# Kernel optimization log

Measured on AMD Instinct MI355X. Metric: run time of the kernel, lower is better.

## Reference

```python
import jax, jax.numpy as jnp
import numpy as np

B, T, D, H = 64, 1024, 64, 128  # batch, time, n_mels, gru hidden


def _gru_dir(xW, Whh, bhh, reverse):
    # xW: [B, T, 3H] precomputed input projection; PyTorch gate order: r, z, n
    def step(h, gi):
        gh = h @ Whh.T + bhh
        i_r, i_z, i_n = jnp.split(gi, 3, axis=-1)
        h_r, h_z, h_n = jnp.split(gh, 3, axis=-1)
        r = jax.nn.sigmoid(i_r + h_r)
        zg = jax.nn.sigmoid(i_z + h_z)
        n = jnp.tanh(i_n + r * h_n)
        h2 = (1.0 - zg) * n + zg * h
        return h2, h2
    h0 = jnp.zeros((xW.shape[0], Whh.shape[1]), xW.dtype)
    _, hs = jax.lax.scan(step, h0, jnp.swapaxes(xW, 0, 1), reverse=reverse)
    return jnp.swapaxes(hs, 0, 1)  # [B, T, H]


def _bigru_layer(x, wih_f, whh_f, bih_f, bhh_f, wih_b, whh_b, bih_b, bhh_b):
    hf = _gru_dir(x @ wih_f.T + bih_f, whh_f, bhh_f, False)
    hb = _gru_dir(x @ wih_b.T + bih_b, whh_b, bhh_b, True)
    return jnp.concatenate([hf, hb], axis=-1)  # [B, T, 2H]


def setup_inputs():
    key = jax.random.key(0)
    ks = jax.random.split(key, 24)
    s = 1.0 / np.sqrt(H)  # PyTorch GRU/Linear-ish uniform init scale

    def p(k, shape):
        return jax.random.uniform(k, shape, jnp.float32, -s, s)

    inp = {}
    inp["x"] = jax.random.normal(ks[0], (B, T, D), jnp.float32)
    inp["motor_k"] = jax.random.randint(ks[1], (B,), 0, 5)  # 0-based motor id
    i = 2
    for l, din in [(0, D), (1, 2 * H)]:
        for d in ("f", "b"):
            inp[f"wih_l{l}{d}"] = p(ks[i], (3 * H, din)); i += 1
            inp[f"whh_l{l}{d}"] = p(ks[i], (3 * H, H)); i += 1
            inp[f"bih_l{l}{d}"] = p(ks[i], (3 * H,)); i += 1
            inp[f"bhh_l{l}{d}"] = p(ks[i], (3 * H,)); i += 1
    inp["attn_w"] = p(ks[i], (1, 2 * H)); i += 1
    inp["attn_b"] = jnp.zeros((1,), jnp.float32)
    inp["motor_w"] = p(ks[i], (5, 2 * H)); i += 1
    inp["motor_b"] = jnp.zeros((5,), jnp.float32)
    inp["state_w"] = p(ks[i], (5, 2, 2 * H)); i += 1  # 5 heads, 2 codes each
    inp["state_b"] = jnp.zeros((5, 2), jnp.float32)
    return inp


def reference(x, motor_k,
              wih_l0f, whh_l0f, bih_l0f, bhh_l0f,
              wih_l0b, whh_l0b, bih_l0b, bhh_l0b,
              wih_l1f, whh_l1f, bih_l1f, bhh_l1f,
              wih_l1b, whh_l1b, bih_l1b, bhh_l1b,
              attn_w, attn_b, motor_w, motor_b, state_w, state_b):
    # bi-GRU, 2 layers (dropout inactive at eval)
    z = _bigru_layer(x, wih_l0f, whh_l0f, bih_l0f, bhh_l0f,
                     wih_l0b, whh_l0b, bih_l0b, bhh_l0b)
    z = _bigru_layer(z, wih_l1f, whh_l1f, bih_l1f, bhh_l1f,
                     wih_l1b, whh_l1b, bih_l1b, bhh_l1b)
    # mean-attention pooling over time
    scores = jnp.einsum('btd,od->bt', z, attn_w) + attn_b[0]
    a = jax.nn.softmax(scores, axis=1)
    pooled = jnp.einsum('btd,bt->bd', z, a)  # [B, 2H]
    logits_motor = pooled @ motor_w.T + motor_b  # [B, 5]
    # per-sample conditional head dispatch (all heads have 2 codes -> Cmax=2)
    Wk = state_w[motor_k]  # [B, 2, 2H]
    bk = state_b[motor_k]  # [B, 2]
    logits_state = jnp.einsum('bd,bcd->bc', pooled, Wk) + bk
    return (logits_motor, logits_state)
```

## Files before the change

kernel.cpp:

```cpp
#include <hip/hip_runtime.h>


typedef unsigned short u16;

__global__ __launch_bounds__(256) void proj_f32(
    const float* __restrict__ A, const float* __restrict__ Wf, const float* __restrict__ Wb,
    const float* __restrict__ bf_, const float* __restrict__ bb_,
    float* __restrict__ gi, int K, int t0f, int t0b, int lTc, int GB)
{
  const int N = 384;
  int Tc = 1 << lTc;
  int dir = blockIdx.z;
  const float* __restrict__ W    = dir ? Wb  : Wf;
  const float* __restrict__ bias = dir ? bb_ : bf_;
  int t0 = dir ? t0b : t0f;
  float* __restrict__ o = gi + (size_t)dir * GB * Tc * N;

  __shared__ float As[32][64];
  __shared__ float Bs[32][64];

  int tid = threadIdx.x;
  int tx = tid & 15, ty = tid >> 4;
  int m0 = blockIdx.x * 64;
  int n0 = blockIdx.y * 64;

  int srow = tid >> 2;
  int scol = (tid & 3) * 8;

  int mlA = m0 + srow;
  size_t gA = (size_t)(mlA >> lTc) * 1024 + t0 + (mlA & (Tc - 1));
  const float* arow = A + gA * K;
  const float* wrow = W + (size_t)(n0 + srow) * K;

  float acc[4][4];
#pragma unroll
  for (int i = 0; i < 4; i++)
#pragma unroll
    for (int j = 0; j < 4; j++) acc[i][j] = 0.f;

  for (int kk = 0; kk < K; kk += 32) {
    float4 a0 = *(const float4*)(arow + kk + scol);
    float4 a1 = *(const float4*)(arow + kk + scol + 4);
    float4 b0 = *(const float4*)(wrow + kk + scol);
    float4 b1 = *(const float4*)(wrow + kk + scol + 4);
    __syncthreads();
    As[scol + 0][srow] = a0.x; As[scol + 1][srow] = a0.y;
    As[scol + 2][srow] = a0.z; As[scol + 3][srow] = a0.w;
    As[scol + 4][srow] = a1.x; As[scol + 5][srow] = a1.y;
    As[scol + 6][srow] = a1.z; As[scol + 7][srow] = a1.w;
    Bs[scol + 0][srow] = b0.x; Bs[scol + 1][srow] = b0.y;
    Bs[scol + 2][srow] = b0.z; Bs[scol + 3][srow] = b0.w;
    Bs[scol + 4][srow] = b1.x; Bs[scol + 5][srow] = b1.y;
    Bs[scol + 6][srow] = b1.z; Bs[scol + 7][srow] = b1.w;
    __syncthreads();
#pragma unroll
    for (int k = 0; k < 32; k++) {
      float4 av = *(const float4*)&As[k][ty * 4];
      float4 bv = *(const float4*)&Bs[k][tx * 4];
      float am[4] = {av.x, av.y, av.z, av.w};
      float bn[4] = {bv.x, bv.y, bv.z, bv.w};
#pragma unroll
      for (int i = 0; i < 4; i++)
#pragma unroll
        for (int j = 0; j < 4; j++) acc[i][j] = fmaf(am[i], bn[j], acc[i][j]);
    }
  }
#pragma unroll
  for (int i = 0; i < 4; i++) {
    size_t m = (size_t)(m0 + ty * 4 + i);
#pragma unroll
    for (int j = 0; j < 4; j++) {
      int n = n0 + tx * 4 + j;
      o[m * N + n] = acc[i][j] + bias[n];
    }
  }
}

__global__ __launch_bounds__(256, 1) void gru_recur(
    const float* __restrict__ whhf, const float* __restrict__ whhb,
    const float* __restrict__ bhhf, const float* __restrict__ bhhb,
    const float* __restrict__ gi, float* __restrict__ zout,
    float* __restrict__ hstate, int t0f, int t0b, int first, int Tc, int GB)
{
  const int H = 128, G = 384;
  int b   = blockIdx.x >> 1;
  int dir = blockIdx.x & 1;
  const float* __restrict__ whh = dir ? whhb : whhf;
  const float* __restrict__ bhh = dir ? bhhb : bhhf;
  int t0 = dir ? t0b : t0f;
  int tid  = threadIdx.x;
  int i    = tid & 127;
  int half = tid >> 7;

  float wr[64], wz[64], wn[64];
  {
    const float* pr = whh + (size_t)i * H + half * 64;
    const float* pz = whh + (size_t)(H + i) * H + half * 64;
    const float* pn = whh + (size_t)(2 * H + i) * H + half * 64;
#pragma unroll
    for (int k = 0; k < 64; k += 4) {
      float4 vr = *(const float4*)(pr + k);
      float4 vz = *(const float4*)(pz + k);
      float4 vn = *(const float4*)(pn + k);
      wr[k] = vr.x; wr[k+1] = vr.y; wr[k+2] = vr.z; wr[k+3] = vr.w;
      wz[k] = vz.x; wz[k+1] = vz.y; wz[k+2] = vz.z; wz[k+3] = vz.w;
      wn[k] = vn.x; wn[k+1] = vn.y; wn[k+2] = vn.z; wn[k+3] = vn.w;
    }
  }
  float br = bhh[i], bz = bhh[H + i], bn = bhh[2 * H + i];

  __shared__ __align__(16) float hbuf[2][128];
  __shared__ float pbuf[128][3];

  float* hs = hstate + (size_t)(dir * GB + b) * H;
  float h = 0.f;
  if (first) {
    if (tid < H) { hbuf[0][tid] = 0.f; hbuf[1][tid] = 0.f; }
  } else {
    if (tid < H) hbuf[0][tid] = hs[tid];
    if (half == 0) h = hs[i];
  }

  const float* girow = gi + ((size_t)dir * GB + b) * Tc * G;
  float r0r = 0, r0z = 0, r0n = 0, r1r = 0, r1z = 0, r1n = 0;
  if (half == 0) {
    int tt0 = dir ? (Tc - 1) : 0;
    int tt1 = dir ? (Tc - 2) : 1;
    r0r = girow[(size_t)tt0 * G + i];
    r0z = girow[(size_t)tt0 * G + H + i];
    r0n = girow[(size_t)tt0 * G + 2 * H + i];
    r1r = girow[(size_t)tt1 * G + i];
    r1z = girow[(size_t)tt1 * G + H + i];
    r1n = girow[(size_t)tt1 * G + 2 * H + i];
  }
  __syncthreads();

  for (int s = 0; s < Tc; s++) {
    int cur = s & 1;
    float n2r = 0, n2z = 0, n2n = 0;
    if (half == 0 && s < Tc - 2) {
      int tt2 = dir ? (Tc - 3 - s) : (s + 2);
      const float* gp = girow + (size_t)tt2 * G;
      n2r = gp[i]; n2z = gp[H + i]; n2n = gp[2 * H + i];
    }
    float ar = 0.f, az = 0.f, an = 0.f;
    const float* hc = &hbuf[cur][half * 64];
#pragma unroll
    for (int k = 0; k < 64; k += 4) {
      float4 hv = *(const float4*)(hc + k);
      ar = fmaf(wr[k], hv.x, ar);   az = fmaf(wz[k], hv.x, az);   an = fmaf(wn[k], hv.x, an);
      ar = fmaf(wr[k+1], hv.y, ar); az = fmaf(wz[k+1], hv.y, az); an = fmaf(wn[k+1], hv.y, an);
      ar = fmaf(wr[k+2], hv.z, ar); az = fmaf(wz[k+2], hv.z, az); an = fmaf(wn[k+2], hv.z, an);
      ar = fmaf(wr[k+3], hv.w, ar); az = fmaf(wz[k+3], hv.w, az); an = fmaf(wn[k+3], hv.w, an);
    }
    if (half == 1) { pbuf[i][0] = ar; pbuf[i][1] = az; pbuf[i][2] = an; }
    __syncthreads();
    if (half == 0) {
      int tt = dir ? (Tc - 1 - s) : s;
      int t_abs = t0 + tt;
      float grh = ar + pbuf[i][0] + br;
      float gzh = az + pbuf[i][1] + bz;
      float gnh = an + pbuf[i][2] + bn;
      float rg = 1.f / (1.f + __expf(-(r0r + grh)));
      float zg = 1.f / (1.f + __expf(-(r0z + gzh)));
      float npre = r0n + rg * gnh;
      float e  = __expf(-2.f * fabsf(npre));
      float nv = (1.f - e) / (1.f + e);
      nv = (npre < 0.f) ? -nv : nv;
      h = nv + zg * (h - nv);
      hbuf[cur ^ 1][i] = h;
      zout[((size_t)b * 1024 + t_abs) * 256 + dir * H + i] = h;
      r0r = r1r; r0z = r1z; r0n = r1n;
      r1r = n2r; r1z = n2z; r1n = n2n;
    }
    __syncthreads();
  }
  if (half == 0) hs[i] = h;
}

__global__ __launch_bounds__(256) void pool_heads(
    const float* __restrict__ z2, const float* __restrict__ attn_w, const float* __restrict__ attn_b,
    const float* __restrict__ motor_w, const float* __restrict__ motor_b,
    const float* __restrict__ state_w, const float* __restrict__ state_b,
    const int* __restrict__ motor_k, float* __restrict__ out, int bbase)
{
  const int T = 1024, D2 = 256;
  int bl = blockIdx.x;
  int babs = bbase + bl;
  const float* Z = z2 + (size_t)bl * T * D2;
  __shared__ float sc[1024];
  __shared__ float red[8];
  __shared__ float pooled[256];
  int tid = threadIdx.x, lane = tid & 63, wv = tid >> 6;

  float aw0 = attn_w[lane],       aw1 = attn_w[64 + lane];
  float aw2 = attn_w[128 + lane], aw3 = attn_w[192 + lane];
  float ab = attn_b[0];
  for (int t = wv; t < T; t += 4) {
    const float* zr = Z + (size_t)t * D2;
    float s = zr[lane] * aw0 + zr[64 + lane] * aw1
            + zr[128 + lane] * aw2 + zr[192 + lane] * aw3;
#pragma unroll
    for (int off = 32; off; off >>= 1) s += __shfl_down(s, off);
    if (lane == 0) sc[t] = s + ab;
  }
  __syncthreads();

  float m = -3.0e38f;
  for (int t = tid; t < T; t += 256) m = fmaxf(m, sc[t]);
#pragma unroll
  for (int off = 32; off; off >>= 1) m = fmaxf(m, __shfl_down(m, off));
  if (lane == 0) red[wv] = m;
  __syncthreads();
  m = fmaxf(fmaxf(red[0], red[1]), fmaxf(red[2], red[3]));
  float sum = 0.f;
  for (int t = tid; t < T; t += 256) { float e = __expf(sc[t] - m); sc[t] = e; sum += e; }
#pragma unroll
  for (int off = 32; off; off >>= 1) sum += __shfl_down(sum, off);
  if (lane == 0) red[4 + wv] = sum;
  __syncthreads();
  float S = red[4] + red[5] + red[6] + red[7];
  float inv = 1.f / S;

  float acc = 0.f;
  for (int t = 0; t < T; t++) acc = fmaf(sc[t], Z[(size_t)t * D2 + tid], acc);
  pooled[tid] = acc * inv;
  __syncthreads();

  int o = tid >> 5, sl = tid & 31;
  if (o < 7) {
    int mk = motor_k[babs];
    const float* wp; float bias;
    if (o < 5) { wp = motor_w + o * D2;                          bias = motor_b[o]; }
    else       { wp = state_w + ((size_t)mk * 2 + (o - 5)) * D2; bias = state_b[mk * 2 + (o - 5)]; }
    float s = 0.f;
    for (int d = sl; d < D2; d += 32) s += pooled[d] * wp[d];
#pragma unroll
    for (int off = 16; off; off >>= 1) s += __shfl_down(s, off);
    if (sl == 0) {
      float v = s + bias;
      if (o < 5) out[babs * 5 + o] = v;
      else       out[320 + babs * 2 + (o - 5)] = v;
    }
  }
}

extern "C" void kernel_launch(void* const* d_in, const int* in_sizes, int n_in,
                              void* d_out, int out_size, void* d_ws, size_t ws_size,
                              hipStream_t stream) {
  const float* x       = (const float*)d_in[0];
  const int*   motor_k = (const int*)d_in[1];
  const float* wih_l0f = (const float*)d_in[2];
  const float* whh_l0f = (const float*)d_in[3];
  const float* bih_l0f = (const float*)d_in[4];
  const float* bhh_l0f = (const float*)d_in[5];
  const float* wih_l0b = (const float*)d_in[6];
  const float* whh_l0b = (const float*)d_in[7];
  const float* bih_l0b = (const float*)d_in[8];
  const float* bhh_l0b = (const float*)d_in[9];
  const float* wih_l1f = (const float*)d_in[10];
  const float* whh_l1f = (const float*)d_in[11];
  const float* bih_l1f = (const float*)d_in[12];
  const float* bhh_l1f = (const float*)d_in[13];
  const float* wih_l1b = (const float*)d_in[14];
  const float* whh_l1b = (const float*)d_in[15];
  const float* bih_l1b = (const float*)d_in[16];
  const float* bhh_l1b = (const float*)d_in[17];
  const float* attn_w  = (const float*)d_in[18];
  const float* attn_b  = (const float*)d_in[19];
  const float* motor_w = (const float*)d_in[20];
  const float* motor_b = (const float*)d_in[21];
  const float* state_w = (const float*)d_in[22];
  const float* state_b = (const float*)d_in[23];

  static const int candGB[9] = {64,32,16,8,4,2,1,1,1};
  static const int candTc[9] = {256,256,256,256,256,256,256,128,64};
  int GB = 1, Tc = 64;
  for (int c = 0; c < 9; c++) {
    size_t nb = (size_t)candGB[c] * 1024 * 256 * 4 * 2
              + (size_t)2 * candGB[c] * candTc[c] * 384 * 4
              + (size_t)2 * candGB[c] * 128 * 4;
    if (nb <= ws_size) { GB = candGB[c]; Tc = candTc[c]; break; }
  }
  int lTc = 31 - __builtin_clz((unsigned)Tc);
  int nc = 1024 / Tc;

  float* z1 = (float*)d_ws;
  float* z2 = z1 + (size_t)GB * 1024 * 256;
  float* gi = z2 + (size_t)GB * 1024 * 256;
  float* hstate = gi + (size_t)2 * GB * Tc * 384;

  dim3 gpb((unsigned)(GB * Tc / 64), 6, 2);
  for (int gb = 0; gb < 64 / GB; gb++) {
    const float* xg = x + (size_t)gb * GB * 1024 * 64;
    for (int c = 0; c < nc; c++) {
      int t0f = c * Tc, t0b = (nc - 1 - c) * Tc;
      proj_f32<<<gpb, 256, 0, stream>>>(xg, wih_l0f, wih_l0b, bih_l0f, bih_l0b,
                                        gi, 64, t0f, t0b, lTc, GB);
      gru_recur<<<2 * GB, 256, 0, stream>>>(whh_l0f, whh_l0b, bhh_l0f, bhh_l0b, gi, z1,
                                            hstate, t0f, t0b, c == 0, Tc, GB);
    }
    for (int c = 0; c < nc; c++) {
      int t0f = c * Tc, t0b = (nc - 1 - c) * Tc;
      proj_f32<<<gpb, 256, 0, stream>>>(z1, wih_l1f, wih_l1b, bih_l1f, bih_l1b,
                                        gi, 256, t0f, t0b, lTc, GB);
      gru_recur<<<2 * GB, 256, 0, stream>>>(whh_l1f, whh_l1b, bhh_l1f, bhh_l1b, gi, z2,
                                            hstate, t0f, t0b, c == 0, Tc, GB);
    }
    pool_heads<<<GB, 256, 0, stream>>>(z2, attn_w, attn_b, motor_w, motor_b,
                                       state_w, state_b, motor_k, (float*)d_out, gb * GB);
  }
}
```

Measured before the change: 2.234 ms.

## Move GRU pipeline to fp16 with MFMA projection and fdot2 recurrence

Converts the input and input-projection weights to fp16 in a preprocessing kernel. The projection GEMM is replaced by an MFMA 16x16x32 f16 kernel, and gi, z1 and z2 are stored as fp16 to halve memory traffic. The recurrence packs Whh into half2 registers, broadcasts h through readlane and uses fdot2. Both directions of a sample are merged into one 512-thread block. All of this reduces arithmetic and bandwidth cost at the price of fp16 rounding in the hidden state and activations, which may affect accuracy over 1024 steps.

Result: slower. 3.050 ms (+36.5%).

```diff
diff --git a/kernel.cpp b/kernel.cpp
--- a/kernel.cpp
+++ b/kernel.cpp
@@ -2,97 +2,95 @@
 
 
 typedef unsigned short u16;
-
-__global__ __launch_bounds__(256) void proj_f32(
-    const float* __restrict__ A, const float* __restrict__ Wf, const float* __restrict__ Wb,
+typedef _Float16 f16;
+typedef f16  h2  __attribute__((ext_vector_type(2)));
+typedef f16  h8  __attribute__((ext_vector_type(8)));
+typedef float fv4 __attribute__((ext_vector_type(4)));
+
+#if defined(__has_builtin)
+#if __has_builtin(__builtin_amdgcn_fdot2)
+#define HAVE_FDOT2 1
+#endif
+#endif
+
+struct Cvt5 { const float* src[5]; unsigned dst[5]; unsigned cum[6]; };
+
+__global__ void cvt_f16(Cvt5 jb, f16* __restrict__ arena, unsigned total) {
+  unsigned stride = gridDim.x * blockDim.x;
+  for (unsigned idx = blockIdx.x * blockDim.x + threadIdx.x; idx < total; idx += stride) {
+    int j = 0;
+    while (idx >= jb.cum[j + 1]) j++;
+    unsigned e = idx - jb.cum[j];
+    arena[jb.dst[j] + e] = (f16)jb.src[j][e];
+  }
+}
+
+__global__ __launch_bounds__(256) void proj_f16(
+    const f16* __restrict__ A, const f16* __restrict__ Wf, const f16* __restrict__ Wb,
     const float* __restrict__ bf_, const float* __restrict__ bb_,
-    float* __restrict__ gi, int K, int t0f, int t0b, int lTc, int GB)
+    f16* __restrict__ gi, int K, int t0f, int t0b, int lTc, int GB)
 {
   const int N = 384;
   int Tc = 1 << lTc;
-  int dir = blockIdx.z;
-  const float* __restrict__ W    = dir ? Wb  : Wf;
+  int dir = blockIdx.y;
+  const f16* __restrict__ W     = dir ? Wb  : Wf;
   const float* __restrict__ bias = dir ? bb_ : bf_;
   int t0 = dir ? t0b : t0f;
-  float* __restrict__ o = gi + (size_t)dir * GB * Tc * N;
-
-  __shared__ float As[32][64];
-  __shared__ float Bs[32][64];
-
-  int tid = threadIdx.x;
-  int tx = tid & 15, ty = tid >> 4;
-  int m0 = blockIdx.x * 64;
-  int n0 = blockIdx.y * 64;
-
-  int srow = tid >> 2;
-  int scol = (tid & 3) * 8;
-
-  int mlA = m0 + srow;
-  size_t gA = (size_t)(mlA >> lTc) * 1024 + t0 + (mlA & (Tc - 1));
-  const float* arow = A + gA * K;
-  const float* wrow = W + (size_t)(n0 + srow) * K;
-
-  float acc[4][4];
-#pragma unroll
-  for (int i = 0; i < 4; i++)
-#pragma unroll
-    for (int j = 0; j < 4; j++) acc[i][j] = 0.f;
+  f16* __restrict__ o = gi + (size_t)dir * GB * Tc * N;
+
+  int lane = threadIdx.x & 63;
+  int wv   = threadIdx.x >> 6;
+  int mbase = blockIdx.x * 64 + wv * 16;
+  int col  = lane & 15;
+  int koff = (lane >> 4) * 8;
+
+  int ml = mbase + col;
+  size_t g = (size_t)(ml >> lTc) * 1024 + t0 + (ml & (Tc - 1));
+  const f16* ap = A + g * K + koff;
+  const f16* wp = W + (size_t)col * K + koff;
+
+  fv4 acc[24];
+#pragma unroll
+  for (int i = 0; i < 24; i++) acc[i] = (fv4){0.f, 0.f, 0.f, 0.f};
 
   for (int kk = 0; kk < K; kk += 32) {
-    float4 a0 = *(const float4*)(arow + kk + scol);
-    float4 a1 = *(const float4*)(arow + kk + scol + 4);
-    float4 b0 = *(const float4*)(wrow + kk + scol);
-    float4 b1 = *(const float4*)(wrow + kk + scol + 4);
-    __syncthreads();
-    As[scol + 0][srow] = a0.x; As[scol + 1][srow] = a0.y;
-    As[scol + 2][srow] = a0.z; As[scol + 3][srow] = a0.w;
-    As[scol + 4][srow] = a1.x; As[scol + 5][srow] = a1.y;
-    As[scol + 6][srow] = a1.z; As[scol + 7][srow] = a1.w;
-    Bs[scol + 0][srow] = b0.x; Bs[scol + 1][srow] = b0.y;
-    Bs[scol + 2][srow] = b0.z; Bs[scol + 3][srow] = b0.w;
-    Bs[scol + 4][srow] = b1.x; Bs[scol + 5][srow] = b1.y;
-    Bs[scol + 6][srow] = b1.z; Bs[scol + 7][srow] = b1.w;
-    __syncthreads();
-#pragma unroll
-    for (int k = 0; k < 32; k++) {
-      float4 av = *(const float4*)&As[k][ty * 4];
-      float4 bv = *(const float4*)&Bs[k][tx * 4];
-      float am[4] = {av.x, av.y, av.z, av.w};
-      float bn[4] = {bv.x, bv.y, bv.z, bv.w};
-#pragma unroll
-      for (int i = 0; i < 4; i++)
-#pragma unroll
-        for (int j = 0; j < 4; j++) acc[i][j] = fmaf(am[i], bn[j], acc[i][j]);
-    }
-  }
-#pragma unroll
-  for (int i = 0; i < 4; i++) {
-    size_t m = (size_t)(m0 + ty * 4 + i);
-#pragma unroll
-    for (int j = 0; j < 4; j++) {
-      int n = n0 + tx * 4 + j;
-      o[m * N + n] = acc[i][j] + bias[n];
-    }
-  }
-}
-
-__global__ __launch_bounds__(256, 1) void gru_recur(
+    h8 a = *(const h8*)(ap + kk);
+#pragma unroll
+    for (int nt = 0; nt < 24; nt++) {
+      h8 bfrag = *(const h8*)(wp + (size_t)nt * 16 * K + kk);
+      acc[nt] = __builtin_amdgcn_mfma_f32_16x16x32_f16(a, bfrag, acc[nt], 0, 0, 0);
+    }
+  }
+  int rowq = (lane >> 4) * 4;
+#pragma unroll
+  for (int nt = 0; nt < 24; nt++) {
+    int n = nt * 16 + col;
+    float bs = bias[n];
+#pragma unroll
+    for (int r = 0; r < 4; r++) {
+      size_t m = (size_t)(mbase + rowq + r);
+      o[m * N + n] = (f16)(acc[nt][r] + bs);
+    }
+  }
+}
+
+__global__ __launch_bounds__(512, 2) void gru_recur(
     const float* __restrict__ whhf, const float* __restrict__ whhb,
     const float* __restrict__ bhhf, const float* __restrict__ bhhb,
-    const float* __restrict__ gi, float* __restrict__ zout,
+    const f16* __restrict__ gi, f16* __restrict__ zout,
     float* __restrict__ hstate, int t0f, int t0b, int first, int Tc, int GB)
 {
   const int H = 128, G = 384;
-  int b   = blockIdx.x >> 1;
-  int dir = blockIdx.x & 1;
+  int tid  = threadIdx.x;
+  int dir  = tid >> 8;
+  int i    = tid & 127;
+  int half = (tid >> 7) & 1;
+  int b    = blockIdx.x;
   const float* __restrict__ whh = dir ? whhb : whhf;
   const float* __restrict__ bhh = dir ? bhhb : bhhf;
   int t0 = dir ? t0b : t0f;
-  int tid  = threadIdx.x;
-  int i    = tid & 127;
-  int half = tid >> 7;
-
-  float wr[64], wz[64], wn[64];
+
+  h2 wr2[32], wz2[32], wn2[32];
   {
     const float* pr = whh + (size_t)i * H + half * 64;
     const float* pz = whh + (size_t)(H + i) * H + half * 64;
@@ -102,27 +100,29 @@
       float4 vr = *(const float4*)(pr + k);
       float4 vz = *(const float4*)(pz + k);
       float4 vn = *(const float4*)(pn + k);
-      wr[k] = vr.x; wr[k+1] = vr.y; wr[k+2] = vr.z; wr[k+3] = vr.w;
-      wz[k] = vz.x; wz[k+1] = vz.y; wz[k+2] = vz.z; wz[k+3] = vz.w;
-      wn[k] = vn.x; wn[k+1] = vn.y; wn[k+2] = vn.z; wn[k+3] = vn.w;
+      wr2[k/2]     = (h2){(f16)vr.x, (f16)vr.y};
+      wr2[k/2 + 1] = (h2){(f16)vr.z, (f16)vr.w};
+      wz2[k/2]     = (h2){(f16)vz.x, (f16)vz.y};
+      wz2[k/2 + 1] = (h2){(f16)vz.z, (f16)vz.w};
+      wn2[k/2]     = (h2){(f16)vn.x, (f16)vn.y};
+      wn2[k/2 + 1] = (h2){(f16)vn.z, (f16)vn.w};
     }
   }
   float br = bhh[i], bz = bhh[H + i], bn = bhh[2 * H + i];
 
-  __shared__ __align__(16) float hbuf[2][128];
-  __shared__ float pbuf[128][3];
+  __shared__ __align__(16) f16 hbuf2[2][2][128];
+  __shared__ float pbuf[2][128][3];
 
   float* hs = hstate + (size_t)(dir * GB + b) * H;
   float h = 0.f;
-  if (first) {
-    if (tid < H) { hbuf[0][tid] = 0.f; hbuf[1][tid] = 0.f; }
-  } else {
-    if (tid < H) hbuf[0][tid] = hs[tid];
-    if (half == 0) h = hs[i];
-  }
-
-  const float* girow = gi + ((size_t)dir * GB + b) * Tc * G;
-  float r0r = 0, r0z = 0, r0n = 0, r1r = 0, r1z = 0, r1n = 0;
+  if (half == 0) {
+    if (!first) h = hs[i];
+    hbuf2[dir][0][i] = (f16)h;
+  }
+
+  const f16* girow = gi + (size_t)(dir * GB + b) * Tc * G;
+  f16 r0r = (f16)0.f, r0z = (f16)0.f, r0n = (f16)0.f;
+  f16 r1r = (f16)0.f, r1z = (f16)0.f, r1n = (f16)0.f;
   if (half == 0) {
     int tt0 = dir ? (Tc - 1) : 0;
     int tt1 = dir ? (Tc - 2) : 1;
@@ -135,41 +135,52 @@
   }
   __syncthreads();
 
+  int lane = tid & 63;
+  const int* hb[2] = { (const int*)&hbuf2[dir][0][0], (const int*)&hbuf2[dir][1][0] };
+  int hidx = half * 32 + (lane & 31);
+
   for (int s = 0; s < Tc; s++) {
     int cur = s & 1;
-    float n2r = 0, n2z = 0, n2n = 0;
+    f16 n2r = (f16)0.f, n2z = (f16)0.f, n2n = (f16)0.f;
     if (half == 0 && s < Tc - 2) {
       int tt2 = dir ? (Tc - 3 - s) : (s + 2);
-      const float* gp = girow + (size_t)tt2 * G;
+      const f16* gp = girow + (size_t)tt2 * G;
       n2r = gp[i]; n2z = gp[H + i]; n2n = gp[2 * H + i];
     }
+    int hv = hb[cur][hidx];
     float ar = 0.f, az = 0.f, an = 0.f;
-    const float* hc = &hbuf[cur][half * 64];
-#pragma unroll
-    for (int k = 0; k < 64; k += 4) {
-      float4 hv = *(const float4*)(hc + k);
-      ar = fmaf(wr[k], hv.x, ar);   az = fmaf(wz[k], hv.x, az);   an = fmaf(wn[k], hv.x, an);
-      ar = fmaf(wr[k+1], hv.y, ar); az = fmaf(wz[k+1], hv.y, az); an = fmaf(wn[k+1], hv.y, an);
-      ar = fmaf(wr[k+2], hv.z, ar); az = fmaf(wz[k+2], hv.z, az); an = fmaf(wn[k+2], hv.z, an);
-      ar = fmaf(wr[k+3], hv.w, ar); az = fmaf(wz[k+3], hv.w, az); an = fmaf(wn[k+3], hv.w, an);
-    }
-    if (half == 1) { pbuf[i][0] = ar; pbuf[i][1] = az; pbuf[i][2] = an; }
+#pragma unroll
+    for (int k = 0; k < 32; k++) {
+      int si = __builtin_amdgcn_readlane(hv, k);
+      h2 sh; __builtin_memcpy(&sh, &si, 4);
+#if HAVE_FDOT2
+      ar = __builtin_amdgcn_fdot2(wr2[k], sh, ar, false);
+      az = __builtin_amdgcn_fdot2(wz2[k], sh, az, false);
+      an = __builtin_amdgcn_fdot2(wn2[k], sh, an, false);
+#else
+      float s0 = (float)sh[0], s1 = (float)sh[1];
+      ar = fmaf((float)wr2[k][0], s0, ar); ar = fmaf((float)wr2[k][1], s1, ar);
+      az = fmaf((float)wz2[k][0], s0, az); az = fmaf((float)wz2[k][1], s1, az);
+      an = fmaf((float)wn2[k][0], s0, an); an = fmaf((float)wn2[k][1], s1, an);
+#endif
+    }
+    if (half == 1) { pbuf[dir][i][0] = ar; pbuf[dir][i][1] = az; pbuf[dir][i][2] = an; }
     __syncthreads();
     if (half == 0) {
       int tt = dir ? (Tc - 1 - s) : s;
       int t_abs = t0 + tt;
-      float grh = ar + pbuf[i][0] + br;
-      float gzh = az + pbuf[i][1] + bz;
-      float gnh = an + pbuf[i][2] + bn;
-      float rg = 1.f / (1.f + __expf(-(r0r + grh)));
-      float zg = 1.f / (1.f + __expf(-(r0z + gzh)));
-      float npre = r0n + rg * gnh;
+      float grh = ar + pbuf[dir][i][0] + br;
+      float gzh = az + pbuf[dir][i][1] + bz;
+      float gnh = an + pbuf[dir][i][2] + bn;
+      float rg = 1.f / (1.f + __expf(-((float)r0r + grh)));
+      float zg = 1.f / (1.f + __expf(-((float)r0z + gzh)));
+      float npre = (float)r0n + rg * gnh;
       float e  = __expf(-2.f * fabsf(npre));
       float nv = (1.f - e) / (1.f + e);
       nv = (npre < 0.f) ? -nv : nv;
       h = nv + zg * (h - nv);
-      hbuf[cur ^ 1][i] = h;
-      zout[((size_t)b * 1024 + t_abs) * 256 + dir * H + i] = h;
+      hbuf2[dir][cur ^ 1][i] = (f16)h;
+      zout[((size_t)b * 1024 + t_abs) * 256 + dir * H + i] = (f16)h;
       r0r = r1r; r0z = r1z; r0n = r1n;
       r1r = n2r; r1z = n2z; r1n = n2n;
     }
@@ -179,7 +190,7 @@
 }
 
 __global__ __launch_bounds__(256) void pool_heads(
-    const float* __restrict__ z2, const float* __restrict__ attn_w, const float* __restrict__ attn_b,
+    const f16* __restrict__ z2, const float* __restrict__ attn_w, const float* __restrict__ attn_b,
     const float* __restrict__ motor_w, const float* __restrict__ motor_b,
     const float* __restrict__ state_w, const float* __restrict__ state_b,
     const int* __restrict__ motor_k, float* __restrict__ out, int bbase)
@@ -187,7 +198,7 @@
   const int T = 1024, D2 = 256;
   int bl = blockIdx.x;
   int babs = bbase + bl;
-  const float* Z = z2 + (size_t)bl * T * D2;
+  const f16* Z = z2 + (size_t)bl * T * D2;
   __shared__ float sc[1024];
   __shared__ float red[8];
   __shared__ float pooled[256];
@@ -197,9 +208,9 @@
   float aw2 = attn_w[128 + lane], aw3 = attn_w[192 + lane];
   float ab = attn_b[0];
   for (int t = wv; t < T; t += 4) {
-    const float* zr = Z + (size_t)t * D2;
-    float s = zr[lane] * aw0 + zr[64 + lane] * aw1
-            + zr[128 + lane] * aw2 + zr[192 + lane] * aw3;
+    const f16* zr = Z + (size_t)t * D2;
+    float s = (float)zr[lane] * aw0 + (float)zr[64 + lane] * aw1
+            + (float)zr[128 + lane] * aw2 + (float)zr[192 + lane] * aw3;
 #pragma unroll
     for (int off = 32; off; off >>= 1) s += __shfl_down(s, off);
     if (lane == 0) sc[t] = s + ab;
@@ -223,7 +234,7 @@
   float inv = 1.f / S;
 
   float acc = 0.f;
-  for (int t = 0; t < T; t++) acc = fmaf(sc[t], Z[(size_t)t * D2 + tid], acc);
+  for (int t = 0; t < T; t++) acc = fmaf(sc[t], (float)Z[(size_t)t * D2 + tid], acc);
   pooled[tid] = acc * inv;
   __syncthreads();
 
@@ -248,21 +259,16 @@
 extern "C" void kernel_launch(void* const* d_in, const int* in_sizes, int n_in,
                               void* d_out, int out_size, void* d_ws, size_t ws_size,
                               hipStream_t stream) {
-  const float* x       = (const float*)d_in[0];
-  const int*   motor_k = (const int*)d_in[1];
-  const float* wih_l0f = (const float*)d_in[2];
+  const int* motor_k = (const int*)d_in[1];
   const float* whh_l0f = (const float*)d_in[3];
   const float* bih_l0f = (const float*)d_in[4];
   const float* bhh_l0f = (const float*)d_in[5];
-  const float* wih_l0b = (const float*)d_in[6];
   const float* whh_l0b = (const float*)d_in[7];
   const float* bih_l0b = (const float*)d_in[8];
   const float* bhh_l0b = (const float*)d_in[9];
-  const float* wih_l1f = (const float*)d_in[10];
   const float* whh_l1f = (const float*)d_in[11];
   const float* bih_l1f = (const float*)d_in[12];
   const float* bhh_l1f = (const float*)d_in[13];
-  const float* wih_l1b = (const float*)d_in[14];
   const float* whh_l1b = (const float*)d_in[15];
   const float* bih_l1b = (const float*)d_in[16];
   const float* bhh_l1b = (const float*)d_in[17];
@@ -273,39 +279,59 @@
   const float* state_w = (const float*)d_in[22];
   const float* state_b = (const float*)d_in[23];
 
+  static const unsigned nel[5] = {4194304, 24576, 24576, 98304, 98304};
+  static const int      idx[5] = {0, 2, 6, 10, 14};
+  Cvt5 jb;
+  unsigned cum = 0;
+  unsigned dst[5];
+  for (int j = 0; j < 5; j++) {
+    jb.src[j] = (const float*)d_in[idx[j]];
+    jb.cum[j] = cum; jb.dst[j] = cum; dst[j] = cum;
+    cum += nel[j];
+  }
+  jb.cum[5] = cum;
+  f16* arena = (f16*)d_ws;
+  size_t dynOffB = ((size_t)cum * 2 + 255) & ~(size_t)255;
+
   static const int candGB[9] = {64,32,16,8,4,2,1,1,1};
   static const int candTc[9] = {256,256,256,256,256,256,256,128,64};
   int GB = 1, Tc = 64;
   for (int c = 0; c < 9; c++) {
-    size_t nb = (size_t)candGB[c] * 1024 * 256 * 4 * 2
-              + (size_t)2 * candGB[c] * candTc[c] * 384 * 4
+    size_t nb = dynOffB
+              + (size_t)candGB[c] * 1024 * 256 * 2 * 2
+              + (size_t)2 * candGB[c] * candTc[c] * 384 * 2
               + (size_t)2 * candGB[c] * 128 * 4;
     if (nb <= ws_size) { GB = candGB[c]; Tc = candTc[c]; break; }
   }
   int lTc = 31 - __builtin_clz((unsigned)Tc);
   int nc = 1024 / Tc;
 
-  float* z1 = (float*)d_ws;
-  float* z2 = z1 + (size_t)GB * 1024 * 256;
-  float* gi = z2 + (size_t)GB * 1024 * 256;
-  float* hstate = gi + (size_t)2 * GB * Tc * 384;
-
-  dim3 gpb((unsigned)(GB * Tc / 64), 6, 2);
+  f16* z1 = (f16*)((char*)d_ws + dynOffB);
+  f16* z2 = z1 + (size_t)GB * 1024 * 256;
+  f16* gi = z2 + (size_t)GB * 1024 * 256;
+  float* hstate = (float*)(gi + (size_t)2 * GB * Tc * 384);
+
+  const f16 *x16 = arena + dst[0], *w0f = arena + dst[1], *w0b = arena + dst[2],
+            *w1f = arena + dst[3], *w1b = arena + dst[4];
+
+  cvt_f16<<<1024, 256, 0, stream>>>(jb, arena, cum);
+
+  dim3 gpb((unsigned)(GB * Tc / 64), 2, 1);
   for (int gb = 0; gb < 64 / GB; gb++) {
-    const float* xg = x + (size_t)gb * GB * 1024 * 64;
+    const f16* xg = x16 + (size_t)gb * GB * 1024 * 64;
     for (int c = 0; c < nc; c++) {
       int t0f = c * Tc, t0b = (nc - 1 - c) * Tc;
-      proj_f32<<<gpb, 256, 0, stream>>>(xg, wih_l0f, wih_l0b, bih_l0f, bih_l0b,
+      proj_f16<<<gpb, 256, 0, stream>>>(xg, w0f, w0b, bih_l0f, bih_l0b,
                                         gi, 64, t0f, t0b, lTc, GB);
-      gru_recur<<<2 * GB, 256, 0, stream>>>(whh_l0f, whh_l0b, bhh_l0f, bhh_l0b, gi, z1,
-                                            hstate, t0f, t0b, c == 0, Tc, GB);
+      gru_recur<<<GB, 512, 0, stream>>>(whh_l0f, whh_l0b, bhh_l0f, bhh_l0b, gi, z1,
+                                        hstate, t0f, t0b, c == 0, Tc, GB);
     }
     for (int c = 0; c < nc; c++) {
       int t0f = c * Tc, t0b = (nc - 1 - c) * Tc;
-      proj_f32<<<gpb, 256, 0, stream>>>(z1, wih_l1f, wih_l1b, bih_l1f, bih_l1b,
+      proj_f16<<<gpb, 256, 0, stream>>>(z1, w1f, w1b, bih_l1f, bih_l1b,
                                         gi, 256, t0f, t0b, lTc, GB);
-      gru_recur<<<2 * GB, 256, 0, stream>>>(whh_l1f, whh_l1b, bhh_l1f, bhh_l1b, gi, z2,
-                                            hstate, t0f, t0b, c == 0, Tc, GB);
+      gru_recur<<<GB, 512, 0, stream>>>(whh_l1f, whh_l1b, bhh_l1f, bhh_l1b, gi, z2,
+                                        hstate, t0f, t0b, c == 0, Tc, GB);
     }
     pool_heads<<<GB, 256, 0, stream>>>(z2, attn_w, attn_b, motor_w, motor_b,
                                        state_w, state_b, motor_k, (float*)d_out, gb * GB);
```
